# Kernel optimization log

Measured on AMD Instinct MI355X. Metric: run time of the kernel, lower is better.

The kernel has to match this reference:

```python
import jax, jax.numpy as jnp
import numpy as np

B, S, D, H = 4, 1024, 1024, 16
DH = D // H
LN_EPS = 1e-5


def setup_inputs() -> dict:
    key = jax.random.key(0)
    ks = jax.random.split(key, 12)
    lim = 1.0 / np.sqrt(D)
    u = lambda k, shp: jax.random.uniform(k, shp, jnp.float32, -lim, lim)
    return {
        "x": jax.random.normal(ks[0], (B, S, D), jnp.float32),
        "Wq": u(ks[1], (D, D)), "bq": u(ks[2], (D,)),
        "Wk": u(ks[3], (D, D)), "bk": u(ks[4], (D,)),
        "Wv": u(ks[5], (D, D)), "bv": u(ks[6], (D,)),
        "Wo": u(ks[7], (D, D)), "bo": u(ks[8], (D,)),
        "gamma": jnp.ones((D,), jnp.float32),
        "beta": jnp.zeros((D,), jnp.float32),
    }


def _layer_norm(x, gamma, beta):
    mu = jnp.mean(x, axis=-1, keepdims=True)
    var = jnp.mean(jnp.square(x - mu), axis=-1, keepdims=True)
    return (x - mu) * jax.lax.rsqrt(var + LN_EPS) * gamma + beta


def reference(x, Wq, bq, Wk, bk, Wv, bv, Wo, bo, gamma, beta):
    # Linear projections (torch Linear: x @ W^T + b)
    Q = x @ Wq.T + bq  # [B, S, D]
    K = x @ Wk.T + bk
    V = x @ Wv.T + bv
    # Faithful to original: raw view(B*H, S, DH) with NO head transpose
    Q = Q.reshape(B * H, S, DH)
    K = K.reshape(B * H, S, DH)
    V = V.reshape(B * H, S, DH)
    scale = DH ** -0.5
    attn = jnp.einsum('bqd,bkd->bqk', Q, K) * scale  # [B*H, S, S]
    attn = jax.nn.softmax(attn, axis=-1)
    ctx = jnp.einsum('bqk,bkd->bqd', attn, V)  # [B*H, S, DH]
    ctx = ctx.reshape(B, S, D)
    out = ctx @ Wo.T + bo
    out = out + x  # residual (dropout p=0.0 is identity)
    return _layer_norm(out, gamma, beta)
```

## Files before the change

kernel.cpp:

```cpp
#include <hip/hip_runtime.h>
#include <hip/hip_bf16.h>


using u16 = unsigned short;
using u32 = unsigned int;
typedef __attribute__((ext_vector_type(8)))  short bf16x8;
typedef __attribute__((ext_vector_type(4)))  float f32x4;
typedef __attribute__((ext_vector_type(16))) float f32x16;
typedef __attribute__((ext_vector_type(4)))  u16  u16x4;
typedef __attribute__((ext_vector_type(8)))  u16  u16x8;

#define AS1C(p) ((const __attribute__((address_space(1))) void*)(p))
#define AS3(p)  ((__attribute__((address_space(3))) void*)(p))

__device__ __forceinline__ u16 f2bf(float f) {
  union { float f; unsigned u; } v; v.f = f;
  unsigned u = v.u;
  return (u16)((u + 0x7fffu + ((u >> 16) & 1u)) >> 16);
}

__device__ __forceinline__ f32x4 mfma16(bf16x8 a, bf16x8 b, f32x4 c) {
  return __builtin_amdgcn_mfma_f32_16x16x32_bf16(a, b, c, 0, 0, 0);
}
__device__ __forceinline__ f32x16 mfma32(bf16x8 a, bf16x8 b, f32x16 c) {
  return __builtin_amdgcn_mfma_f32_32x32x16_bf16(a, b, c, 0, 0, 0);
}

__global__ __launch_bounds__(256) void prep_kernel(
    const float* __restrict__ x,
    const float* __restrict__ wq, const float* __restrict__ wk,
    const float* __restrict__ wv, const float* __restrict__ wo,
    const float* __restrict__ bq, const float* __restrict__ bk, const float* __restrict__ bv,
    u16* __restrict__ xb, u16* __restrict__ wb, float* __restrict__ bc)
{
  int ch = blockIdx.x * 256 + threadIdx.x;
  if (ch < 2097152) {
    const float* src; u16* dst;
    if (ch < 1048576) { src = x + ch * 4; dst = xb + ch * 4; }
    else {
      int c2 = ch - 1048576;
      int wsel = c2 >> 18;
      int off  = c2 & 262143;
      const float* wsrc[4] = { wq, wk, wv, wo };
      src = wsrc[wsel] + off * 4;
      dst = wb + wsel * 1048576 + off * 4;
    }
    f32x4 v = *(const f32x4*)src;
    u16x4 o;
    o[0] = f2bf(v[0]); o[1] = f2bf(v[1]); o[2] = f2bf(v[2]); o[3] = f2bf(v[3]);
    *(u16x4*)dst = o;
  } else {
    int c3 = ch - 2097152;
    int bsel = c3 >> 8, off = c3 & 255;
    const float* bsrc[3] = { bq, bk, bv };
    f32x4 v = *(const f32x4*)(bsrc[bsel] + off * 4);
    *(f32x4*)(bc + bsel * 1024 + off * 4) = v;
  }
}

__global__ __launch_bounds__(256) void gemm_qkv(
    const u16* __restrict__ A, const u16* __restrict__ Bw,
    const float* __restrict__ bias, u16* __restrict__ outb)
{
  __shared__ u16 As[3][4096];
  __shared__ u16 Bs[3][4096];

  const int K = 1024;
  int tid = threadIdx.x, w = tid >> 6, lane = tid & 63;
  int g = lane >> 4, lr = lane & 15;
  int wr = w >> 1, wcn = w & 1;

  int bid = blockIdx.x;
  int bm = (bid & 7) + 8 * ((bid >> 3) & 3);
  int bn = bid >> 5;

  int ch0 = tid, ch1 = tid + 256;
  auto srcoff = [&](int ch) -> size_t {
    int r = ch >> 2, pc = ch & 3;
    int gc = pc ^ ((r >> 2) & 3);
    return (size_t)r * K + gc * 8;
  };
  const u16* aS0 = A  + (size_t)(bm * 128) * K + srcoff(ch0);
  const u16* aS1 = A  + (size_t)(bm * 128) * K + srcoff(ch1);
  const u16* bS0 = Bw + (size_t)(bn * 128) * K + srcoff(ch0);
  const u16* bS1 = Bw + (size_t)(bn * 128) * K + srcoff(ch1);
  int lo0 = ch0 * 8, lo1 = ch1 * 8;

  auto STAGE = [&](int buf, int kt) {
    __builtin_amdgcn_global_load_lds(AS1C(aS0 + kt * 32), AS3(&As[buf][lo0]), 16, 0, 0);
    __builtin_amdgcn_global_load_lds(AS1C(aS1 + kt * 32), AS3(&As[buf][lo1]), 16, 0, 0);
    __builtin_amdgcn_global_load_lds(AS1C(bS0 + kt * 32), AS3(&Bs[buf][lo0]), 16, 0, 0);
    __builtin_amdgcn_global_load_lds(AS1C(bS1 + kt * 32), AS3(&Bs[buf][lo1]), 16, 0, 0);
  };

  f32x4 acc[4][4] = {};
  int pc8 = (g ^ ((lr >> 2) & 3)) * 8;

  auto COMPUTE = [&](int buf) {
    bf16x8 af[4], bfr[4];
#pragma unroll
    for (int m = 0; m < 4; ++m)
      af[m] = *(const bf16x8*)&As[buf][(wr * 64 + m * 16 + lr) * 32 + pc8];
#pragma unroll
    for (int n = 0; n < 4; ++n)
      bfr[n] = *(const bf16x8*)&Bs[buf][(wcn * 64 + n * 16 + lr) * 32 + pc8];
    __builtin_amdgcn_s_setprio(1);
#pragma unroll
    for (int m = 0; m < 4; ++m)
#pragma unroll
      for (int n = 0; n < 4; ++n)
        acc[m][n] = mfma16(af[m], bfr[n], acc[m][n]);
    __builtin_amdgcn_s_setprio(0);
  };

  STAGE(0, 0); STAGE(1, 1);

  int sb = 2, cb = 0;
  for (int t = 0; t < 31; ++t) {
    asm volatile("s_waitcnt vmcnt(4)" ::: "memory");
    __builtin_amdgcn_s_barrier();
    asm volatile("" ::: "memory");
    if (t < 30) {
      STAGE(sb, t + 2);
      if (++sb == 3) sb = 0;
    }
    COMPUTE(cb);
    if (++cb == 3) cb = 0;
  }
  asm volatile("s_waitcnt vmcnt(0)" ::: "memory");
  __builtin_amdgcn_s_barrier();
  asm volatile("" ::: "memory");
  COMPUTE(cb);

#pragma unroll
  for (int m = 0; m < 4; ++m) {
    int row0 = bm * 128 + wr * 64 + m * 16 + 4 * g;
#pragma unroll
    for (int n = 0; n < 4; ++n) {
      int col = bn * 128 + wcn * 64 + n * 16 + lr;
#pragma unroll
      for (int i = 0; i < 4; ++i) {
        float v = acc[m][n][i] + bias[col];
        int r = row0 + i;
        if (col < 1024) {
          outb[(size_t)r * 1024 + col] = f2bf(v * 0.125f);
        } else if (col < 2048) {
          outb[4194304 + (size_t)r * 1024 + (col - 1024)] = f2bf(v);
        } else {
          int c = col - 2048;
          outb[8388608 + (size_t)(r >> 6) * 65536 + (size_t)(c & 63) * 1024
               + (r & 63) * 16 + (c >> 6)] = f2bf(v);
        }
      }
    }
  }
}

__global__ __launch_bounds__(256) void gemm_op(
    const u16* __restrict__ A, const u16* __restrict__ Bw,
    const float* __restrict__ bias, const float* __restrict__ resid,
    float* __restrict__ outf)
{
  __shared__ u16 As[3][2048];
  __shared__ u16 Bs[3][4096];

  const int K = 1024;
  int tid = threadIdx.x, w = tid >> 6, lane = tid & 63;
  int g = lane >> 4, lr = lane & 15;
  int wr = w >> 1, wcn = w & 1;
  int bid = blockIdx.x;
  int bm = bid & 63, bn = bid >> 6;

  auto srcoff = [&](int ch) -> size_t {
    int r = ch >> 2, pc = ch & 3;
    int gc = pc ^ ((r >> 2) & 3);
    return (size_t)r * K + gc * 8;
  };
  const u16* aS0 = A  + (size_t)(bm * 64)  * K + srcoff(tid);
  const u16* bS0 = Bw + (size_t)(bn * 128) * K + srcoff(tid);
  const u16* bS1 = Bw + (size_t)(bn * 128) * K + srcoff(tid + 256);

  auto STAGE = [&](int buf, int kt) {
    __builtin_amdgcn_global_load_lds(AS1C(aS0 + kt * 32), AS3(&As[buf][tid * 8]),        16, 0, 0);
    __builtin_amdgcn_global_load_lds(AS1C(bS0 + kt * 32), AS3(&Bs[buf][tid * 8]),        16, 0, 0);
    __builtin_amdgcn_global_load_lds(AS1C(bS1 + kt * 32), AS3(&Bs[buf][2048 + tid * 8]), 16, 0, 0);
  };

  f32x4 acc[2][4] = {};
  int pc8 = (g ^ ((lr >> 2) & 3)) * 8;

  auto COMPUTE = [&](int buf) {
    bf16x8 af[2], bfr[4];
#pragma unroll
    for (int m = 0; m < 2; ++m)
      af[m] = *(const bf16x8*)&As[buf][(wr * 32 + m * 16 + lr) * 32 + pc8];
#pragma unroll
    for (int n = 0; n < 4; ++n)
      bfr[n] = *(const bf16x8*)&Bs[buf][(wcn * 64 + n * 16 + lr) * 32 + pc8];
    __builtin_amdgcn_s_setprio(1);
#pragma unroll
    for (int m = 0; m < 2; ++m)
#pragma unroll
      for (int n = 0; n < 4; ++n)
        acc[m][n] = mfma16(af[m], bfr[n], acc[m][n]);
    __builtin_amdgcn_s_setprio(0);
  };

  STAGE(0, 0); STAGE(1, 1);

  int sb = 2, cb = 0;
  for (int t = 0; t < 31; ++t) {
    asm volatile("s_waitcnt vmcnt(3)" ::: "memory");
    __builtin_amdgcn_s_barrier();
    asm volatile("" ::: "memory");
    if (t < 30) {
      STAGE(sb, t + 2);
      if (++sb == 3) sb = 0;
    }
    COMPUTE(cb);
    if (++cb == 3) cb = 0;
  }
  asm volatile("s_waitcnt vmcnt(0)" ::: "memory");
  __builtin_amdgcn_s_barrier();
  asm volatile("" ::: "memory");
  COMPUTE(cb);

#pragma unroll
  for (int m = 0; m < 2; ++m) {
    int row0 = bm * 64 + wr * 32 + m * 16 + 4 * g;
#pragma unroll
    for (int n = 0; n < 4; ++n) {
      int col = bn * 128 + wcn * 64 + n * 16 + lr;
#pragma unroll
      for (int i = 0; i < 4; ++i) {
        size_t idx = (size_t)(row0 + i) * 1024 + col;
        outf[idx] = acc[m][n][i] + bias[col] + resid[idx];
      }
    }
  }
}

__global__ __launch_bounds__(128) void attn_kernel(
    const u16* __restrict__ Qb, const u16* __restrict__ Kb,
    const u16* __restrict__ Vtb, u16* __restrict__ Ob)
{
  __shared__ u16 Ks[2][4096];
  __shared__ u16 Vts[2][4096];

  int blk = blockIdx.x;
  int bh = blk & 63, qt = blk >> 6;
  int tid = threadIdx.x, wid = tid >> 6, lane = tid & 63;
  int l31 = lane & 31, hi = lane >> 5;

  const u16* Qp = Qb  + (size_t)bh * 65536;
  const u16* Kp = Kb  + (size_t)bh * 65536;
  const u16* Vp = Vtb + (size_t)bh * 65536;

  int q = qt * 64 + wid * 32 + l31;

  bf16x8 qf[4];
#pragma unroll
  for (int s = 0; s < 4; ++s)
    qf[s] = *(const bf16x8*)&Qp[(size_t)q * 64 + s * 16 + hi * 8];

  f32x16 oacc[2] = {};
  float mrow = -3e38f, lrow = 0.f;

  const u16* gk[4]; const u16* gv[4];
#pragma unroll
  for (int j = 0; j < 4; ++j) {
    int ch = tid + 128 * j;
    int kc = ch >> 3, scc = ch & 7;
    int sc = scc ^ (kc & 7);
    gk[j] = Kp + (size_t)kc * 64   + sc * 8;
    gv[j] = Vp + (size_t)kc * 1024 + sc * 8;
  }

#define STAGE_A(b, kt) do { \
  _Pragma("unroll") \
  for (int j = 0; j < 4; ++j) { \
    int ch = tid + 128 * j; \
    __builtin_amdgcn_global_load_lds(AS1C(gk[j] + (size_t)(kt) * 4096), AS3(&Ks[b][ch * 8]),  16, 0, 0); \
    __builtin_amdgcn_global_load_lds(AS1C(gv[j] + (kt) * 64),           AS3(&Vts[b][ch * 8]), 16, 0, 0); \
  } } while (0)

  STAGE_A(0, 0);
  __syncthreads();
  int cur = 0;

  for (int kt = 0; kt < 16; ++kt) {
    if (kt + 1 < 16) STAGE_A(cur ^ 1, kt + 1);

    f32x16 s2[2];
#pragma unroll
    for (int ks = 0; ks < 2; ++ks) {
      f32x16 z = {};
      int row = ks * 32 + l31;
      int rx = (row & 7);
#pragma unroll
      for (int s = 0; s < 4; ++s) {
        bf16x8 kb = *(const bf16x8*)&Ks[cur][row * 64 + (((2 * s + hi) ^ rx) * 8)];
        z = mfma32(kb, qf[s], z);
      }
      s2[ks] = z;
    }

    float tv[16];
#pragma unroll
    for (int r = 0; r < 16; ++r) tv[r] = fmaxf(s2[0][r], s2[1][r]);
#pragma unroll
    for (int st = 8; st > 0; st >>= 1)
#pragma unroll
      for (int r = 0; r < st; ++r) tv[r] = fmaxf(tv[r], tv[r + st]);
    float tm = fmaxf(tv[0], __shfl_xor(tv[0], 32));
    float mn = fmaxf(mrow, tm);
    float corr = __expf(mrow - mn);

    float sv[16];
#pragma unroll
    for (int r = 0; r < 16; ++r) {
      s2[0][r] = __expf(s2[0][r] - mn);
      s2[1][r] = __expf(s2[1][r] - mn);
      sv[r] = s2[0][r] + s2[1][r];
    }
#pragma unroll
    for (int st = 8; st > 0; st >>= 1)
#pragma unroll
      for (int r = 0; r < st; ++r) sv[r] += sv[r + st];
    float rs = sv[0] + __shfl_xor(sv[0], 32);
    lrow = lrow * corr + rs;
    mrow = mn;

#pragma unroll
    for (int dt = 0; dt < 2; ++dt)
#pragma unroll
      for (int r = 0; r < 16; ++r) oacc[dt][r] *= corr;

    u32 wpk[2][4][2];
#pragma unroll
    for (int ks = 0; ks < 2; ++ks)
#pragma unroll
      for (int r1 = 0; r1 < 4; ++r1)
#pragma unroll
        for (int p = 0; p < 2; ++p)
          wpk[ks][r1][p] = (u32)f2bf(s2[ks][4 * r1 + 2 * p])
                         | ((u32)f2bf(s2[ks][4 * r1 + 2 * p + 1]) << 16);

#pragma unroll
    for (int s = 0; s < 4; ++s) {
      int ks = s >> 1, t = s & 1;
      u32 a0 = wpk[ks][2 * t][0],     a1 = wpk[ks][2 * t][1];
      u32 b0 = wpk[ks][2 * t + 1][0], b1 = wpk[ks][2 * t + 1][1];
      u32 sa0 = (u32)__shfl_xor((int)a0, 32), sa1 = (u32)__shfl_xor((int)a1, 32);
      u32 sb0 = (u32)__shfl_xor((int)b0, 32), sb1 = (u32)__shfl_xor((int)b1, 32);
      union { u32 u[4]; bf16x8 v; } pb;
      pb.u[0] = hi ? sb0 : a0;
      pb.u[1] = hi ? sb1 : a1;
      pb.u[2] = hi ? b0 : sa0;
      pb.u[3] = hi ? b1 : sa1;
#pragma unroll
      for (int dt = 0; dt < 2; ++dt) {
        int row = dt * 32 + l31;
        bf16x8 vb = *(const bf16x8*)&Vts[cur][row * 64 + (((2 * s + hi) ^ (row & 7)) * 8)];
        oacc[dt] = mfma32(vb, pb.v, oacc[dt]);
      }
    }

    __syncthreads();
    cur ^= 1;
  }

  float inv = 1.f / lrow;
  u16* Op = Ob + (size_t)bh * 65536 + (size_t)q * 64;
#pragma unroll
  for (int dt = 0; dt < 2; ++dt)
#pragma unroll
    for (int rq = 0; rq < 4; ++rq) {
      int d0 = dt * 32 + 8 * rq + 4 * hi;
      u16x4 o4;
#pragma unroll
      for (int rr = 0; rr < 4; ++rr) o4[rr] = f2bf(oacc[dt][4 * rq + rr] * inv);
      *(u16x4*)&Op[d0] = o4;
    }
}

__global__ __launch_bounds__(256) void ln_kernel(
    float* __restrict__ out, const float* __restrict__ gamma, const float* __restrict__ beta)
{
  int row = blockIdx.x, tid = threadIdx.x;
  int lane = tid & 63, wid = tid >> 6;
  f32x4 v = *(const f32x4*)&out[(size_t)row * 1024 + tid * 4];
  float s = v[0] + v[1] + v[2] + v[3];
  float q = v[0] * v[0] + v[1] * v[1] + v[2] * v[2] + v[3] * v[3];
#pragma unroll
  for (int ms = 1; ms < 64; ms <<= 1) { s += __shfl_xor(s, ms); q += __shfl_xor(q, ms); }
  __shared__ float red[8];
  if (lane == 0) { red[wid] = s; red[wid + 4] = q; }
  __syncthreads();
  s = red[0] + red[1] + red[2] + red[3];
  q = red[4] + red[5] + red[6] + red[7];
  float mu = s * (1.f / 1024.f);
  float var = q * (1.f / 1024.f) - mu * mu;
  float inv = rsqrtf(var + 1e-5f);
  f32x4 g4 = *(const f32x4*)&gamma[tid * 4];
  f32x4 b4 = *(const f32x4*)&beta[tid * 4];
  f32x4 o;
#pragma unroll
  for (int j = 0; j < 4; ++j) o[j] = (v[j] - mu) * inv * g4[j] + b4[j];
  *(f32x4*)&out[(size_t)row * 1024 + tid * 4] = o;
}

extern "C" void kernel_launch(void* const* d_in, const int* in_sizes, int n_in,
                              void* d_out, int out_size, void* d_ws, size_t ws_size,
                              hipStream_t stream) {
  const float* x     = (const float*)d_in[0];
  const float* Wq    = (const float*)d_in[1];
  const float* bq    = (const float*)d_in[2];
  const float* Wk    = (const float*)d_in[3];
  const float* bk    = (const float*)d_in[4];
  const float* Wv    = (const float*)d_in[5];
  const float* bv    = (const float*)d_in[6];
  const float* Wo    = (const float*)d_in[7];
  const float* bo    = (const float*)d_in[8];
  const float* gamma = (const float*)d_in[9];
  const float* beta  = (const float*)d_in[10];
  float* out = (float*)d_out;

  char* ws = (char*)d_ws;
  u16*   xb  = (u16*)ws;
  u16*   wb  = (u16*)(ws + (8u << 20));
  float* bc  = (float*)(ws + (16u << 20));
  u16*   qkv = (u16*)(ws + (16u << 20) + 16384);
  u16*   ctx = xb;

  prep_kernel<<<8195, 256, 0, stream>>>(x, Wq, Wk, Wv, Wo, bq, bk, bv, xb, wb, bc);

  gemm_qkv<<<768, 256, 0, stream>>>(xb, wb, bc, qkv);

  attn_kernel<<<1024, 128, 0, stream>>>(qkv, qkv + 4194304, qkv + 8388608, ctx);

  gemm_op<<<512, 256, 0, stream>>>(ctx, wb + 3 * 1048576, bo, x, out);

  ln_kernel<<<4096, 256, 0, stream>>>(out, gamma, beta);
}
```

Before: 134.3 us.

## Triple-buffer attention K/V, widen blocks to 256 threads, skip lazy softmax rescale

The attention kernel now uses 256-thread blocks covering 128 queries, so each staged K/V tile is shared by more waves and only half as many blocks are launched. The double-buffered loop with a full __syncthreads at the end is replaced by a three-stage ring with one waitcnt and barrier per iteration. The online softmax skips the rescale whenever every lane's new max exceeds the running max by at most 8, which removes the exp and the accumulator multiply in most iterations. The GEMM kernels also drop their s_setprio hints around the MFMA loops. Costs are higher LDS use per block and a bounded growth of exponentials that could lose precision in bf16.

```diff
diff --git a/kernel.cpp b/kernel.cpp
--- a/kernel.cpp
+++ b/kernel.cpp
@@ -104,13 +104,11 @@
 #pragma unroll
     for (int n = 0; n < 4; ++n)
       bfr[n] = *(const bf16x8*)&Bs[buf][(wcn * 64 + n * 16 + lr) * 32 + pc8];
-    __builtin_amdgcn_s_setprio(1);
 #pragma unroll
     for (int m = 0; m < 4; ++m)
 #pragma unroll
       for (int n = 0; n < 4; ++n)
         acc[m][n] = mfma16(af[m], bfr[n], acc[m][n]);
-    __builtin_amdgcn_s_setprio(0);
   };
 
   STAGE(0, 0); STAGE(1, 1);
@@ -197,13 +195,11 @@
 #pragma unroll
     for (int n = 0; n < 4; ++n)
       bfr[n] = *(const bf16x8*)&Bs[buf][(wcn * 64 + n * 16 + lr) * 32 + pc8];
-    __builtin_amdgcn_s_setprio(1);
 #pragma unroll
     for (int m = 0; m < 2; ++m)
 #pragma unroll
       for (int n = 0; n < 4; ++n)
         acc[m][n] = mfma16(af[m], bfr[n], acc[m][n]);
-    __builtin_amdgcn_s_setprio(0);
   };
 
   STAGE(0, 0); STAGE(1, 1);
@@ -240,12 +236,12 @@
   }
 }
 
-__global__ __launch_bounds__(128) void attn_kernel(
+__global__ __launch_bounds__(256) void attn_kernel(
     const u16* __restrict__ Qb, const u16* __restrict__ Kb,
     const u16* __restrict__ Vtb, u16* __restrict__ Ob)
 {
-  __shared__ u16 Ks[2][4096];
-  __shared__ u16 Vts[2][4096];
+  __shared__ u16 Ks[3][4096];
+  __shared__ u16 Vts[3][4096];
 
   int blk = blockIdx.x;
   int bh = blk & 63, qt = blk >> 6;
@@ -256,7 +252,7 @@
   const u16* Kp = Kb  + (size_t)bh * 65536;
   const u16* Vp = Vtb + (size_t)bh * 65536;
 
-  int q = qt * 64 + wid * 32 + l31;
+  int q = qt * 128 + wid * 32 + l31;
 
   bf16x8 qf[4];
 #pragma unroll
@@ -266,30 +262,37 @@
   f32x16 oacc[2] = {};
   float mrow = -3e38f, lrow = 0.f;
 
-  const u16* gk[4]; const u16* gv[4];
-#pragma unroll
-  for (int j = 0; j < 4; ++j) {
-    int ch = tid + 128 * j;
+  const u16* gk[2]; const u16* gv[2];
+#pragma unroll
+  for (int j = 0; j < 2; ++j) {
+    int ch = tid + 256 * j;
     int kc = ch >> 3, scc = ch & 7;
     int sc = scc ^ (kc & 7);
     gk[j] = Kp + (size_t)kc * 64   + sc * 8;
     gv[j] = Vp + (size_t)kc * 1024 + sc * 8;
   }
 
-#define STAGE_A(b, kt) do { \
-  _Pragma("unroll") \
-  for (int j = 0; j < 4; ++j) { \
-    int ch = tid + 128 * j; \
-    __builtin_amdgcn_global_load_lds(AS1C(gk[j] + (size_t)(kt) * 4096), AS3(&Ks[b][ch * 8]),  16, 0, 0); \
-    __builtin_amdgcn_global_load_lds(AS1C(gv[j] + (kt) * 64),           AS3(&Vts[b][ch * 8]), 16, 0, 0); \
-  } } while (0)
-
-  STAGE_A(0, 0);
-  __syncthreads();
-  int cur = 0;
-
+  auto STAGE = [&](int buf, int kt) {
+#pragma unroll
+    for (int j = 0; j < 2; ++j) {
+      int ch = tid + 256 * j;
+      __builtin_amdgcn_global_load_lds(AS1C(gk[j] + (size_t)kt * 4096), AS3(&Ks[buf][ch * 8]),  16, 0, 0);
+      __builtin_amdgcn_global_load_lds(AS1C(gv[j] + kt * 64),           AS3(&Vts[buf][ch * 8]), 16, 0, 0);
+    }
+  };
+
+  STAGE(0, 0); STAGE(1, 1);
+
+  int sb = 2, cb = 0;
   for (int kt = 0; kt < 16; ++kt) {
-    if (kt + 1 < 16) STAGE_A(cur ^ 1, kt + 1);
+    if (kt < 15) { asm volatile("s_waitcnt vmcnt(4)" ::: "memory"); }
+    else         { asm volatile("s_waitcnt vmcnt(0)" ::: "memory"); }
+    __builtin_amdgcn_s_barrier();
+    asm volatile("" ::: "memory");
+    if (kt < 14) {
+      STAGE(sb, kt + 2);
+      if (++sb == 3) sb = 0;
+    }
 
     f32x16 s2[2];
 #pragma unroll
@@ -299,7 +302,7 @@
       int rx = (row & 7);
 #pragma unroll
       for (int s = 0; s < 4; ++s) {
-        bf16x8 kb = *(const bf16x8*)&Ks[cur][row * 64 + (((2 * s + hi) ^ rx) * 8)];
+        bf16x8 kb = *(const bf16x8*)&Ks[cb][row * 64 + (((2 * s + hi) ^ rx) * 8)];
         z = mfma32(kb, qf[s], z);
       }
       s2[ks] = z;
@@ -313,8 +316,11 @@
 #pragma unroll
       for (int r = 0; r < st; ++r) tv[r] = fmaxf(tv[r], tv[r + st]);
     float tm = fmaxf(tv[0], __shfl_xor(tv[0], 32));
-    float mn = fmaxf(mrow, tm);
-    float corr = __expf(mrow - mn);
+
+    bool nores = __all(tm - mrow <= 8.0f);
+    float mn, corr;
+    if (nores) { mn = mrow; corr = 1.f; }
+    else       { mn = fmaxf(mrow, tm); corr = __expf(mrow - mn); }
 
     float sv[16];
 #pragma unroll
@@ -328,13 +334,17 @@
 #pragma unroll
       for (int r = 0; r < st; ++r) sv[r] += sv[r + st];
     float rs = sv[0] + __shfl_xor(sv[0], 32);
-    lrow = lrow * corr + rs;
-    mrow = mn;
-
-#pragma unroll
-    for (int dt = 0; dt < 2; ++dt)
-#pragma unroll
-      for (int r = 0; r < 16; ++r) oacc[dt][r] *= corr;
+
+    if (nores) {
+      lrow += rs;
+    } else {
+#pragma unroll
+      for (int dt = 0; dt < 2; ++dt)
+#pragma unroll
+        for (int r = 0; r < 16; ++r) oacc[dt][r] *= corr;
+      lrow = lrow * corr + rs;
+      mrow = mn;
+    }
 
     u32 wpk[2][4][2];
 #pragma unroll
@@ -361,13 +371,12 @@
 #pragma unroll
       for (int dt = 0; dt < 2; ++dt) {
         int row = dt * 32 + l31;
-        bf16x8 vb = *(const bf16x8*)&Vts[cur][row * 64 + (((2 * s + hi) ^ (row & 7)) * 8)];
+        bf16x8 vb = *(const bf16x8*)&Vts[cb][row * 64 + (((2 * s + hi) ^ (row & 7)) * 8)];
         oacc[dt] = mfma32(vb, pb.v, oacc[dt]);
       }
     }
 
-    __syncthreads();
-    cur ^= 1;
+    if (++cb == 3) cb = 0;
   }
 
   float inv = 1.f / lrow;
@@ -437,7 +446,7 @@
 
   gemm_qkv<<<768, 256, 0, stream>>>(xb, wb, bc, qkv);
 
-  attn_kernel<<<1024, 128, 0, stream>>>(qkv, qkv + 4194304, qkv + 8388608, ctx);
+  attn_kernel<<<512, 256, 0, stream>>>(qkv, qkv + 4194304, qkv + 8388608, ctx);
 
   gemm_op<<<512, 256, 0, stream>>>(ctx, wb + 3 * 1048576, bo, x, out);
 
```

Result: slower. 150.5 us (+12.1%).
